# Kernel tuning notes

Hardware: AMD Instinct MI355X
Metric: run time of the kernel (lower is better)

The kernel has to match this reference:

```python
import jax, jax.numpy as jnp
import numpy as np
from jax import lax


def _conv(x, w, b, pad):
    y = lax.conv_general_dilated(x, w, (1, 1), [(pad, pad), (pad, pad)],
                                 dimension_numbers=('NCHW', 'OIHW', 'NCHW'))
    return y + b[None, :, None, None]


def setup_inputs() -> dict:
    key = jax.random.key(0)
    ks = jax.random.split(key, 16)
    B, H, W = 8, 1024, 1024

    def wt(k, shape):
        fan = int(np.prod(shape[1:]))
        return jax.random.normal(k, shape, jnp.float32) / np.sqrt(fan)

    return {
        'x': jax.random.uniform(ks[0], (B, 3, H, W), jnp.float32),
        'w1': wt(ks[1], (3, 3, 1, 1)),  'b1': 0.05 * jax.random.normal(ks[2], (3,), jnp.float32),
        'w2': wt(ks[3], (3, 3, 3, 3)),  'b2': 0.05 * jax.random.normal(ks[4], (3,), jnp.float32),
        'w3': wt(ks[5], (3, 6, 5, 5)),  'b3': 0.05 * jax.random.normal(ks[6], (3,), jnp.float32),
        'w4': wt(ks[7], (3, 6, 7, 7)),  'b4': 0.05 * jax.random.normal(ks[8], (3,), jnp.float32),
        'w5': wt(ks[9], (3, 12, 3, 3)), 'b5': 0.05 * jax.random.normal(ks[10], (3,), jnp.float32),
        'rw1': wt(ks[11], (8, 3, 3, 3)), 'rb1': 0.05 * jax.random.normal(ks[12], (8,), jnp.float32),
        'rw2': wt(ks[13], (3, 8, 3, 3)), 'rb2': 0.05 * jax.random.normal(ks[14], (3,), jnp.float32),
    }


def reference(x, w1, b1, w2, b2, w3, b3, w4, b4, w5, b5, rw1, rb1, rw2, rb2):
    B, _, H, W = x.shape
    relu = jax.nn.relu
    x = jnp.clip(x, 0.0, 1.0)
    original = x

    # K-estimation trunk
    x1 = relu(_conv(x, w1, b1, 0))
    x2 = relu(_conv(x1, w2, b2, 1))
    x3 = relu(_conv(jnp.concatenate([x1, x2], 1), w3, b3, 2))
    x4 = relu(_conv(jnp.concatenate([x2, x3], 1), w4, b4, 3))
    k = relu(_conv(jnp.concatenate([x1, x2, x3, x4], 1), w5, b5, 1))
    k = jnp.clip(k, 0.05, 2.0)

    bright = x.mean(axis=1).reshape(B, -1)           # [B, HW]
    nb = max(int(H * W * 0.001), 1)
    _, idx = lax.top_k(bright, nb)                   # [B, nb]
    flat_img = x.transpose(0, 2, 3, 1).reshape(B, -1, 3)
    A = jnp.take_along_axis(flat_img, idx[:, :, None], axis=1).mean(axis=1)  # [B,3]
    overall = x.mean(axis=(1, 2, 3))
    A = A * jnp.clip(1.2 - overall, 0.8, 1.5)[:, None]
    A = jnp.clip(A, 0.5, 0.95)[:, :, None, None]     # [B,3,1,1]

    # Adaptive transmission and scene radiance recovery
    brightness = x.mean(axis=1, keepdims=True)
    strength = jnp.clip(1.0 - brightness, 0.3, 0.8)
    t = jnp.clip(1.0 - strength * k, 0.1, 1.0)
    J = (x - A) / (t + 1e-5) + A
    J = jnp.nan_to_num(J, nan=0.5, posinf=1.0, neginf=0.0)

    # refinement residual
    refined = _conv(relu(_conv(J, rw1, rb1, 1)), rw2, rb2, 1)
    result = J + 0.2 * refined

    # 'guided filter' loop: the window means are computed but unused; the
    # actual output is a 50/50 blend with the original input.
    result = 0.5 * result + 0.5 * original

    # Histogram equalization per (image, channel) with 256 bins over [0,1]
    ch = result.reshape(B * 3, H * W)
    valid = ((ch >= 0.0) & (ch <= 1.0)).astype(ch.dtype)   # histc ignores out-of-range
    bins = jnp.clip(jnp.floor(ch * 256.0).astype(jnp.int32), 0, 255)
    hist = jax.vmap(lambda b_, v_: jnp.zeros((256,), ch.dtype).at[b_].add(v_))(bins, valid)
    cdf = jnp.cumsum(hist, axis=1)
    lut = jnp.clip(cdf / cdf[:, -1:], 0.0, 1.0)            # [B*3, 256]
    lidx = jnp.clip((ch * 255.0).astype(jnp.int32), 0, 255)
    result = jnp.take_along_axis(lut, lidx, axis=1).reshape(B, 3, H, W)

    # Per-channel contrast stretch
    mn = result.min(axis=(2, 3), keepdims=True)
    mx = result.max(axis=(2, 3), keepdims=True)
    stretch = (result - mn) / jnp.maximum(mx - mn, 0.05) * 0.95
    result = jnp.where(mx - mn > 0.05, stretch, result)

    # Saturation boost + soft contrast curve
    mean_color = result.mean(axis=1, keepdims=True)
    result = mean_color + 1.3 * (result - mean_color)
    result = jax.nn.sigmoid((result - 0.5) * 5.0) * 0.95 + 0.025
    return jnp.clip(result, 0.0, 1.0)
```

## Files before the change

kernel.cpp:

```cpp
#include <hip/hip_runtime.h>
#include <math.h>

#define NBATCH 8
#define IH 1024
#define IW 1024
#define HW (IH*IW)
#define NTOP 1048
#define TIE_CAP 4096

#define TTS 18
#define TD1 (TTS+14)
#define TD2 (TTS+12)
#define TD3 (TTS+8)
#define TD4 (TTS+2)
#define SD1 33
#define SD2 31
#define SD3 27
#define SD4 21
#define CH1 (SD1*TD1+4)
#define CH2 (SD2*TD2+4)
#define CH3 (SD3*TD3+4)
#define CH4 (SD4*TD4+4)

#define RTS 32
#define RD1 (RTS+4)
#define RD2 (RTS+2)

__device__ __forceinline__ float clip01(float v){ return fminf(fmaxf(v, 0.f), 1.f); }

template<int CH,int SD,int KS,int CIN>
__device__ __forceinline__ void accrow4(float a[3][4], const float (*sx)[CH],
    int base, const float* __restrict__ w, int ci0)
{
#pragma unroll 1
  for (int ci = 0; ci < 3; ++ci) {
#pragma unroll 1
    for (int ky = 0; ky < KS; ++ky) {
      float v[KS+3];
      const float* row = &sx[ci][base + ky*SD];
#pragma unroll
      for (int j = 0; j < KS+3; ++j) v[j] = row[j];
#pragma unroll
      for (int o = 0; o < 3; ++o) {
        const float* wp = w + ((o*CIN + ci0+ci)*KS + ky)*KS;
#pragma unroll
        for (int kx = 0; kx < KS; ++kx) {
          float wv = wp[kx];
#pragma unroll
          for (int q = 0; q < 4; ++q)
            a[o][q] = fmaf(v[kx+q], wv, a[o][q]);
        }
      }
    }
  }
}

__global__ void k_init(unsigned* hr, unsigned* prefix, unsigned* remain,
                       float* overall, unsigned* tie_cnt, float* sum_gt,
                       unsigned* histeq, unsigned* mnb, unsigned* mxb)
{
  int t = threadIdx.x;
  for (int i = t; i < 4*NBATCH*256; i += 256) hr[i] = 0u;
  for (int i = t; i < NBATCH*3*256; i += 256) histeq[i] = 0u;
  if (t < NBATCH) { prefix[t] = 0u; remain[t] = NTOP; overall[t] = 0.f; tie_cnt[t] = 0u; }
  if (t < NBATCH*3) { sum_gt[t] = 0.f; mnb[t] = 0x7f7fffffu; mxb[t] = 0u; }
}

__global__ __launch_bounds__(256) void k_bright(const float* __restrict__ x,
    float* __restrict__ bright, float* __restrict__ overall)
{
  __shared__ float sred[256];
  const int b = blockIdx.y;
  const int t = threadIdx.x;
  const float4* c0 = (const float4*)(x + (size_t)b*3*HW);
  const float4* c1 = (const float4*)(x + (size_t)b*3*HW + HW);
  const float4* c2 = (const float4*)(x + (size_t)b*3*HW + 2*(size_t)HW);
  float4* bp = (float4*)(bright + (size_t)b*HW);
  float lsum = 0.f;
  int stride = gridDim.x*blockDim.x;
  for (int i = blockIdx.x*blockDim.x + t; i < HW/4; i += stride) {
    float4 a = c0[i], d = c1[i], e = c2[i];
    float4 br;
    br.x = (clip01(a.x)+clip01(d.x)+clip01(e.x))/3.f;
    br.y = (clip01(a.y)+clip01(d.y)+clip01(e.y))/3.f;
    br.z = (clip01(a.z)+clip01(d.z)+clip01(e.z))/3.f;
    br.w = (clip01(a.w)+clip01(d.w)+clip01(e.w))/3.f;
    bp[i] = br;
    lsum += br.x+br.y+br.z+br.w;
  }
  sred[t] = lsum; __syncthreads();
  for (int s = 128; s > 0; s >>= 1) { if (t < s) sred[t] += sred[t+s]; __syncthreads(); }
  if (t == 0) atomicAdd(&overall[b], sred[0]);
}

__global__ __launch_bounds__(256) void k_trunk(const float* __restrict__ x,
    const float* __restrict__ w1, const float* __restrict__ b1,
    const float* __restrict__ w2, const float* __restrict__ b2,
    const float* __restrict__ w3, const float* __restrict__ b3,
    const float* __restrict__ w4, const float* __restrict__ b4,
    const float* __restrict__ w5, const float* __restrict__ b5,
    float* __restrict__ kout)
{
  __shared__ float s1[3][CH1];
  __shared__ float s2[3][CH2];
  __shared__ float s3[3][CH3];
  __shared__ float s4[3][CH4];
  const int b = blockIdx.z;
  const int gy0 = blockIdx.y*TTS, gx0 = blockIdx.x*TTS;
  const float* xb = x + (size_t)b*3*HW;
  const int tid = threadIdx.x;

  for (int idx = tid; idx < TD1*TD1; idx += 256) {
    int iy = idx/TD1, ix = idx - iy*TD1;
    int gy = gy0 - 7 + iy, gx = gx0 - 7 + ix;
    float o0 = 0.f, o1 = 0.f, o2 = 0.f;
    if (gy >= 0 && gy < IH && gx >= 0 && gx < IW) {
      int gi = gy*IW + gx;
      float c0 = clip01(xb[gi]), c1 = clip01(xb[HW+gi]), c2 = clip01(xb[2*HW+gi]);
      o0 = fmaxf(fmaf(w1[0],c0,fmaf(w1[1],c1,fmaf(w1[2],c2,b1[0]))), 0.f);
      o1 = fmaxf(fmaf(w1[3],c0,fmaf(w1[4],c1,fmaf(w1[5],c2,b1[1]))), 0.f);
      o2 = fmaxf(fmaf(w1[6],c0,fmaf(w1[7],c1,fmaf(w1[8],c2,b1[2]))), 0.f);
    }
    int off = iy*SD1 + ix;
    s1[0][off]=o0; s1[1][off]=o1; s1[2][off]=o2;
  }
  __syncthreads();

  {
    const int NU = ((TD2+3)/4)*TD2;
    int u = tid;
    if (u < NU) {
      int iy = u % TD2, ix0 = (u / TD2)*4;
      int gy = gy0 - 6 + iy;
      float a[3][4];
#pragma unroll
      for (int o=0;o<3;++o){float bv=b2[o];a[o][0]=bv;a[o][1]=bv;a[o][2]=bv;a[o][3]=bv;}
      accrow4<CH1,SD1,3,3>(a, s1, iy*SD1 + ix0, w2, 0);
      bool rowok = (gy >= 0 && gy < IH);
#pragma unroll
      for (int q=0;q<4;++q) {
        int ix = ix0+q;
        if (ix < TD2) {
          int gx = gx0 - 6 + ix;
          bool ok = rowok && gx >= 0 && gx < IW;
          int off = iy*SD2 + ix;
          s2[0][off] = ok ? fmaxf(a[0][q],0.f) : 0.f;
          s2[1][off] = ok ? fmaxf(a[1][q],0.f) : 0.f;
          s2[2][off] = ok ? fmaxf(a[2][q],0.f) : 0.f;
        }
      }
    }
  }
  __syncthreads();

  {
    const int NU = ((TD3+3)/4)*TD3;
    int u = tid;
    if (u < NU) {
      int iy = u % TD3, ix0 = (u / TD3)*4;
      int gy = gy0 - 4 + iy;
      float a[3][4];
#pragma unroll
      for (int o=0;o<3;++o){float bv=b3[o];a[o][0]=bv;a[o][1]=bv;a[o][2]=bv;a[o][3]=bv;}
      accrow4<CH1,SD1,5,6>(a, s1, (iy+1)*SD1 + (ix0+1), w3, 0);
      accrow4<CH2,SD2,5,6>(a, s2, iy*SD2 + ix0,         w3, 3);
      bool rowok = (gy >= 0 && gy < IH);
#pragma unroll
      for (int q=0;q<4;++q) {
        int ix = ix0+q;
        if (ix < TD3) {
          int gx = gx0 - 4 + ix;
          bool ok = rowok && gx >= 0 && gx < IW;
          int off = iy*SD3 + ix;
          s3[0][off] = ok ? fmaxf(a[0][q],0.f) : 0.f;
          s3[1][off] = ok ? fmaxf(a[1][q],0.f) : 0.f;
          s3[2][off] = ok ? fmaxf(a[2][q],0.f) : 0.f;
        }
      }
    }
  }
  __syncthreads();

  {
    const int NU = ((TD4+3)/4)*TD4;
    int u = tid;
    if (u < NU) {
      int iy = u % TD4, ix0 = (u / TD4)*4;
      int gy = gy0 - 1 + iy;
      float a[3][4];
#pragma unroll
      for (int o=0;o<3;++o){float bv=b4[o];a[o][0]=bv;a[o][1]=bv;a[o][2]=bv;a[o][3]=bv;}
      accrow4<CH2,SD2,7,6>(a, s2, (iy+2)*SD2 + (ix0+2), w4, 0);
      accrow4<CH3,SD3,7,6>(a, s3, iy*SD3 + ix0,         w4, 3);
      bool rowok = (gy >= 0 && gy < IH);
#pragma unroll
      for (int q=0;q<4;++q) {
        int ix = ix0+q;
        if (ix < TD4) {
          int gx = gx0 - 1 + ix;
          bool ok = rowok && gx >= 0 && gx < IW;
          int off = iy*SD4 + ix;
          s4[0][off] = ok ? fmaxf(a[0][q],0.f) : 0.f;
          s4[1][off] = ok ? fmaxf(a[1][q],0.f) : 0.f;
          s4[2][off] = ok ? fmaxf(a[2][q],0.f) : 0.f;
        }
      }
    }
  }
  __syncthreads();

  {
    const int NU = ((TTS+3)/4)*TTS;
    int u = tid;
    if (u < NU) {
      int iy = u % TTS, ix0 = (u / TTS)*4;
      int gy = gy0 + iy;
      float a[3][4];
#pragma unroll
      for (int o=0;o<3;++o){float bv=b5[o];a[o][0]=bv;a[o][1]=bv;a[o][2]=bv;a[o][3]=bv;}
      accrow4<CH1,SD1,3,12>(a, s1, (iy+6)*SD1 + (ix0+6), w5, 0);
      accrow4<CH2,SD2,3,12>(a, s2, (iy+5)*SD2 + (ix0+5), w5, 3);
      accrow4<CH3,SD3,3,12>(a, s3, (iy+3)*SD3 + (ix0+3), w5, 6);
      accrow4<CH4,SD4,3,12>(a, s4, iy*SD4 + ix0,         w5, 9);
      if (gy < IH) {
#pragma unroll
        for (int q=0;q<4;++q) {
          int ix = ix0+q;
          int gx = gx0 + ix;
          if (ix < TTS && gx < IW) {
            size_t gi = (size_t)gy*IW + gx;
            kout[((size_t)b*3+0)*HW + gi] = fminf(fmaxf(a[0][q], 0.05f), 2.0f);
            kout[((size_t)b*3+1)*HW + gi] = fminf(fmaxf(a[1][q], 0.05f), 2.0f);
            kout[((size_t)b*3+2)*HW + gi] = fminf(fmaxf(a[2][q], 0.05f), 2.0f);
          }
        }
      }
    }
  }
}

__global__ __launch_bounds__(256) void k_radix_hist(const float* __restrict__ bright,
    const unsigned* __restrict__ prefix, unsigned* __restrict__ hr, int pass)
{
  __shared__ unsigned lh[256];
  const int b = blockIdx.y;
  const int t = threadIdx.x;
  lh[t] = 0u; __syncthreads();
  const unsigned pf = prefix[b];
  const unsigned mask = (pass == 0) ? 0u : (0xFFFFFFFFu << (32 - 8*pass));
  const int shift = 24 - 8*pass;
  const float* br = bright + (size_t)b*HW;
  int stride = gridDim.x*blockDim.x;
  for (int i = blockIdx.x*blockDim.x + t; i < HW; i += stride) {
    unsigned bits = __float_as_uint(br[i]);
    if ((bits & mask) == pf) atomicAdd(&lh[(bits >> shift) & 0xFFu], 1u);
  }
  __syncthreads();
  if (lh[t]) atomicAdd(&hr[(pass*NBATCH + b)*256 + t], lh[t]);
}

__global__ void k_radix_scan(const unsigned* __restrict__ hr,
    unsigned* __restrict__ prefix, unsigned* __restrict__ remain, int pass)
{
  int b = threadIdx.x;
  if (b >= NBATCH) return;
  unsigned rem = remain[b];
  const unsigned* h = hr + (pass*NBATCH + b)*256;
  const int shift = 24 - 8*pass;
  for (int bin = 255; bin >= 0; --bin) {
    unsigned c = h[bin];
    if (rem <= c) { prefix[b] |= ((unsigned)bin) << shift; remain[b] = rem; return; }
    rem -= c;
  }
  remain[b] = rem;
}

__global__ __launch_bounds__(256) void k_gather(const float* __restrict__ x,
    const float* __restrict__ bright, const unsigned* __restrict__ prefix,
    float* __restrict__ sum_gt, unsigned* __restrict__ tie_cnt, unsigned* __restrict__ tie_idx)
{
  const int b = blockIdx.y;
  const unsigned T = prefix[b];
  const float* br = bright + (size_t)b*HW;
  int stride = gridDim.x*blockDim.x;
  for (int i = blockIdx.x*blockDim.x + threadIdx.x; i < HW; i += stride) {
    unsigned bits = __float_as_uint(br[i]);
    if (bits > T) {
#pragma unroll
      for (int c = 0; c < 3; ++c)
        atomicAdd(&sum_gt[b*3+c], clip01(x[((size_t)b*3+c)*HW + i]));
    } else if (bits == T) {
      unsigned p = atomicAdd(&tie_cnt[b], 1u);
      if (p < TIE_CAP) tie_idx[b*TIE_CAP + p] = i;
    }
  }
}

__global__ __launch_bounds__(256) void k_afinal(const float* __restrict__ x,
    const float* __restrict__ sum_gt, const unsigned* __restrict__ tie_cnt,
    const unsigned* __restrict__ tie_idx, const unsigned* __restrict__ remain,
    const float* __restrict__ overall, float* __restrict__ A)
{
  __shared__ unsigned sidx[TIE_CAP];
  __shared__ unsigned sred[256];
  __shared__ float ssum[3];
  const int b = blockIdx.x;
  const int t = threadIdx.x;
  unsigned cnt = tie_cnt[b]; if (cnt > TIE_CAP) cnt = TIE_CAP;
  unsigned need = remain[b]; if (need > cnt) need = cnt;
  if (t < 3) ssum[t] = 0.f;
  for (unsigned i = t; i < cnt; i += 256) sidx[i] = tie_idx[b*TIE_CAP + i];
  __syncthreads();
  if (need == cnt) {
    float l0=0.f,l1=0.f,l2=0.f;
    for (unsigned i = t; i < cnt; i += 256) {
      unsigned px = sidx[i];
      l0 += clip01(x[((size_t)b*3+0)*HW + px]);
      l1 += clip01(x[((size_t)b*3+1)*HW + px]);
      l2 += clip01(x[((size_t)b*3+2)*HW + px]);
    }
    atomicAdd(&ssum[0], l0); atomicAdd(&ssum[1], l1); atomicAdd(&ssum[2], l2);
    __syncthreads();
  } else {
    for (unsigned it = 0; it < need; ++it) {
      unsigned lmin = 0xFFFFFFFFu;
      for (unsigned i = t; i < cnt; i += 256) lmin = min(lmin, sidx[i]);
      sred[t] = lmin; __syncthreads();
      for (int s = 128; s > 0; s >>= 1) { if (t < s) sred[t] = min(sred[t], sred[t+s]); __syncthreads(); }
      unsigned mv = sred[0];
      if (t == 0) {
        ssum[0] += clip01(x[((size_t)b*3+0)*HW + mv]);
        ssum[1] += clip01(x[((size_t)b*3+1)*HW + mv]);
        ssum[2] += clip01(x[((size_t)b*3+2)*HW + mv]);
      }
      for (unsigned i = t; i < cnt; i += 256) if (sidx[i] == mv) sidx[i] = 0xFFFFFFFFu;
      __syncthreads();
    }
  }
  __syncthreads();
  if (t < 3) {
    float a = (sum_gt[b*3+t] + ssum[t]) / (float)NTOP;
    float f = fminf(fmaxf(1.2f - overall[b]/(float)HW, 0.8f), 1.5f);
    A[b*3+t] = fminf(fmaxf(a*f, 0.5f), 0.95f);
  }
}

__global__ __launch_bounds__(256) void k_refineJ(const float* __restrict__ x,
    const float* __restrict__ kin, const float* __restrict__ A,
    const float* __restrict__ rw1, const float* __restrict__ rb1,
    const float* __restrict__ rw2, const float* __restrict__ rb2,
    float* __restrict__ out)
{
  __shared__ float sJ[3][RD1*RD1];
  __shared__ float sH[8][RD2*RD2];
  const int b = blockIdx.z;
  const int gy0 = blockIdx.y*RTS, gx0 = blockIdx.x*RTS;
  const int tid = threadIdx.x;
  const float A0 = A[b*3+0], A1 = A[b*3+1], A2 = A[b*3+2];
  const float* xb = x + (size_t)b*3*HW;
  const float* kb = kin + (size_t)b*3*HW;

  for (int idx = tid; idx < RD1*RD1; idx += 256) {
    int iy = idx/RD1, ix = idx - iy*RD1;
    int gy = gy0 - 2 + iy, gx = gx0 - 2 + ix;
    float j0 = 0.f, j1 = 0.f, j2 = 0.f;
    if (gy >= 0 && gy < IH && gx >= 0 && gx < IW) {
      size_t gi = (size_t)gy*IW + gx;
      float c0 = clip01(xb[gi]), c1 = clip01(xb[HW+gi]), c2 = clip01(xb[2*(size_t)HW+gi]);
      float br = (c0+c1+c2)/3.f;
      float st = fminf(fmaxf(1.f-br, 0.3f), 0.8f);
      float t0 = fminf(fmaxf(1.f-st*kb[gi],             0.1f),1.f)+1e-5f;
      float t1 = fminf(fmaxf(1.f-st*kb[HW+gi],          0.1f),1.f)+1e-5f;
      float t2 = fminf(fmaxf(1.f-st*kb[2*(size_t)HW+gi],0.1f),1.f)+1e-5f;
      j0 = (c0-A0)/t0 + A0;
      j1 = (c1-A1)/t1 + A1;
      j2 = (c2-A2)/t2 + A2;
    }
    sJ[0][idx]=j0; sJ[1][idx]=j1; sJ[2][idx]=j2;
  }
  __syncthreads();

  for (int idx = tid; idx < RD2*RD2; idx += 256) {
    int iy = idx/RD2, ix = idx - iy*RD2;
    int gy = gy0 - 1 + iy, gx = gx0 - 1 + ix;
    float acc[8];
#pragma unroll
    for (int o = 0; o < 8; ++o) acc[o] = rb1[o];
    if (gy >= 0 && gy < IH && gx >= 0 && gx < IW) {
#pragma unroll
      for (int ci = 0; ci < 3; ++ci) {
#pragma unroll
        for (int ky = 0; ky < 3; ++ky) {
#pragma unroll
          for (int kx = 0; kx < 3; ++kx) {
            float v = sJ[ci][(iy+ky)*RD1 + ix+kx];
#pragma unroll
            for (int o = 0; o < 8; ++o)
              acc[o] = fmaf(v, rw1[((o*3+ci)*3+ky)*3+kx], acc[o]);
          }
        }
      }
#pragma unroll
      for (int o = 0; o < 8; ++o) sH[o][idx] = fmaxf(acc[o], 0.f);
    } else {
#pragma unroll
      for (int o = 0; o < 8; ++o) sH[o][idx] = 0.f;
    }
  }
  __syncthreads();

  for (int idx = tid; idx < RTS*RTS; idx += 256) {
    int iy = idx/RTS, ix = idx - iy*RTS;
    int gy = gy0 + iy, gx = gx0 + ix;
    float r0 = rb2[0], r1 = rb2[1], r2 = rb2[2];
#pragma unroll
    for (int ci = 0; ci < 8; ++ci) {
#pragma unroll
      for (int ky = 0; ky < 3; ++ky) {
#pragma unroll
        for (int kx = 0; kx < 3; ++kx) {
          float v = sH[ci][(iy+ky)*RD2 + ix+kx];
          r0 = fmaf(v, rw2[((0*8+ci)*3+ky)*3+kx], r0);
          r1 = fmaf(v, rw2[((1*8+ci)*3+ky)*3+kx], r1);
          r2 = fmaf(v, rw2[((2*8+ci)*3+ky)*3+kx], r2);
        }
      }
    }
    size_t gi = (size_t)gy*IW + gx;
    float j0 = sJ[0][(iy+2)*RD1 + ix+2];
    float j1 = sJ[1][(iy+2)*RD1 + ix+2];
    float j2 = sJ[2][(iy+2)*RD1 + ix+2];
    out[((size_t)b*3+0)*HW + gi] = 0.5f*(j0 + 0.2f*r0) + 0.5f*clip01(xb[gi]);
    out[((size_t)b*3+1)*HW + gi] = 0.5f*(j1 + 0.2f*r1) + 0.5f*clip01(xb[HW+gi]);
    out[((size_t)b*3+2)*HW + gi] = 0.5f*(j2 + 0.2f*r2) + 0.5f*clip01(xb[2*(size_t)HW+gi]);
  }
}

__global__ __launch_bounds__(256) void k_hist(const float* __restrict__ r, unsigned* __restrict__ hist)
{
  __shared__ unsigned lh[256];
  const int slice = blockIdx.y;
  const int t = threadIdx.x;
  lh[t] = 0u; __syncthreads();
  const float4* p = (const float4*)(r + (size_t)slice*HW);
  int stride = gridDim.x*blockDim.x;
  for (int i = blockIdx.x*blockDim.x + t; i < HW/4; i += stride) {
    float4 v = p[i];
    float a[4] = {v.x, v.y, v.z, v.w};
#pragma unroll
    for (int q = 0; q < 4; ++q) {
      float vv = a[q];
      if (vv >= 0.f && vv <= 1.f) {
        int bin = (int)floorf(vv*256.f);
        bin = min(max(bin, 0), 255);
        atomicAdd(&lh[bin], 1u);
      }
    }
  }
  __syncthreads();
  if (lh[t]) atomicAdd(&hist[slice*256 + t], lh[t]);
}

__global__ void k_cdf(const unsigned* __restrict__ hist, float* __restrict__ lut)
{
  __shared__ float sc[256];
  const int s = blockIdx.x;
  const int t = threadIdx.x;
  sc[t] = (float)hist[s*256 + t];
  __syncthreads();
  for (int off = 1; off < 256; off <<= 1) {
    float add = (t >= off) ? sc[t-off] : 0.f;
    __syncthreads();
    sc[t] += add;
    __syncthreads();
  }
  float total = sc[255];
  lut[s*256 + t] = fminf(fmaxf(sc[t]/total, 0.f), 1.f);
}

__global__ __launch_bounds__(256) void k_apply(float* r, const float* __restrict__ lut,
    unsigned* __restrict__ mnb, unsigned* __restrict__ mxb)
{
  __shared__ float slut[256];
  __shared__ float smn[256], smx[256];
  const int slice = blockIdx.y;
  const int t = threadIdx.x;
  slut[t] = lut[slice*256 + t];
  __syncthreads();
  float lmn = 3.4e38f, lmx = -3.4e38f;
  float4* p = (float4*)(r + (size_t)slice*HW);
  int stride = gridDim.x*blockDim.x;
  for (int i = blockIdx.x*blockDim.x + t; i < HW/4; i += stride) {
    float4 v = p[i];
    float o0 = slut[min(max((int)(v.x*255.f), 0), 255)];
    float o1 = slut[min(max((int)(v.y*255.f), 0), 255)];
    float o2 = slut[min(max((int)(v.z*255.f), 0), 255)];
    float o3 = slut[min(max((int)(v.w*255.f), 0), 255)];
    lmn = fminf(lmn, fminf(fminf(o0,o1), fminf(o2,o3)));
    lmx = fmaxf(lmx, fmaxf(fmaxf(o0,o1), fmaxf(o2,o3)));
    float4 ov = {o0,o1,o2,o3};
    p[i] = ov;
  }
  smn[t] = lmn; smx[t] = lmx; __syncthreads();
  for (int s = 128; s > 0; s >>= 1) {
    if (t < s) { smn[t] = fminf(smn[t], smn[t+s]); smx[t] = fmaxf(smx[t], smx[t+s]); }
    __syncthreads();
  }
  if (t == 0) {
    atomicMin(&mnb[slice], __float_as_uint(smn[0]));
    atomicMax(&mxb[slice], __float_as_uint(smx[0]));
  }
}

__global__ __launch_bounds__(256) void k_final(float* r,
    const unsigned* __restrict__ mnb, const unsigned* __restrict__ mxb)
{
  const int b = blockIdx.y;
  float mn[3], mx[3];
#pragma unroll
  for (int c = 0; c < 3; ++c) { mn[c] = __uint_as_float(mnb[b*3+c]); mx[c] = __uint_as_float(mxb[b*3+c]); }
  int stride = gridDim.x*blockDim.x;
  for (int i = blockIdx.x*blockDim.x + threadIdx.x; i < HW/4; i += stride) {
    float4 v[3];
#pragma unroll
    for (int c = 0; c < 3; ++c) v[c] = ((const float4*)(r + ((size_t)b*3+c)*HW))[i];
    float* f0 = (float*)&v[0]; float* f1 = (float*)&v[1]; float* f2 = (float*)&v[2];
#pragma unroll
    for (int q = 0; q < 4; ++q) {
      float rr[3] = { f0[q], f1[q], f2[q] };
#pragma unroll
      for (int c = 0; c < 3; ++c) {
        float d = mx[c] - mn[c];
        if (d > 0.05f) rr[c] = (rr[c] - mn[c]) / fmaxf(d, 0.05f) * 0.95f;
      }
      float m = (rr[0] + rr[1] + rr[2]) / 3.f;
#pragma unroll
      for (int c = 0; c < 3; ++c) {
        float s = m + 1.3f*(rr[c] - m);
        float o = 1.f/(1.f + expf(-(s - 0.5f)*5.f))*0.95f + 0.025f;
        rr[c] = clip01(o);
      }
      f0[q] = rr[0]; f1[q] = rr[1]; f2[q] = rr[2];
    }
#pragma unroll
    for (int c = 0; c < 3; ++c) ((float4*)(r + ((size_t)b*3+c)*HW))[i] = v[c];
  }
}

extern "C" void kernel_launch(void* const* d_in, const int* in_sizes, int n_in,
                              void* d_out, int out_size, void* d_ws, size_t ws_size,
                              hipStream_t stream) {
  const float* x   = (const float*)d_in[0];
  const float* w1  = (const float*)d_in[1];  const float* b1 = (const float*)d_in[2];
  const float* w2  = (const float*)d_in[3];  const float* b2 = (const float*)d_in[4];
  const float* w3  = (const float*)d_in[5];  const float* b3 = (const float*)d_in[6];
  const float* w4  = (const float*)d_in[7];  const float* b4 = (const float*)d_in[8];
  const float* w5  = (const float*)d_in[9];  const float* b5 = (const float*)d_in[10];
  const float* rw1 = (const float*)d_in[11]; const float* rb1 = (const float*)d_in[12];
  const float* rw2 = (const float*)d_in[13]; const float* rb2 = (const float*)d_in[14];
  float* out = (float*)d_out;

  float* ws = (float*)d_ws;
  float* kbuf   = ws;
  float* bright = kbuf + (size_t)NBATCH*3*HW;
  float* overall = bright + (size_t)NBATCH*HW;
  float* sum_gt  = overall + NBATCH;
  float* Abuf    = sum_gt + NBATCH*3;
  float* lut     = Abuf + NBATCH*3;
  unsigned* hr      = (unsigned*)(lut + NBATCH*3*256);
  unsigned* prefix  = hr + 4*NBATCH*256;
  unsigned* remain  = prefix + NBATCH;
  unsigned* tie_cnt = remain + NBATCH;
  unsigned* tie_idx = tie_cnt + NBATCH;
  unsigned* histeq  = tie_idx + NBATCH*TIE_CAP;
  unsigned* mnb     = histeq + NBATCH*3*256;
  unsigned* mxb     = mnb + NBATCH*3;

  k_init<<<1, 256, 0, stream>>>(hr, prefix, remain, overall, tie_cnt, sum_gt, histeq, mnb, mxb);
  k_bright<<<dim3(1024, NBATCH), 256, 0, stream>>>(x, bright, overall);
  k_trunk<<<dim3((IW+TTS-1)/TTS, (IH+TTS-1)/TTS, NBATCH), 256, 0, stream>>>(
      x, w1, b1, w2, b2, w3, b3, w4, b4, w5, b5, kbuf);
  for (int p = 0; p < 4; ++p) {
    k_radix_hist<<<dim3(64, NBATCH), 256, 0, stream>>>(bright, prefix, hr, p);
    k_radix_scan<<<1, 64, 0, stream>>>(hr, prefix, remain, p);
  }
  k_gather<<<dim3(128, NBATCH), 256, 0, stream>>>(x, bright, prefix, sum_gt, tie_cnt, tie_idx);
  k_afinal<<<NBATCH, 256, 0, stream>>>(x, sum_gt, tie_cnt, tie_idx, remain, overall, Abuf);
  k_refineJ<<<dim3(IW/RTS, IH/RTS, NBATCH), 256, 0, stream>>>(
      x, kbuf, Abuf, rw1, rb1, rw2, rb2, out);
  k_hist<<<dim3(64, NBATCH*3), 256, 0, stream>>>(out, histeq);
  k_cdf<<<NBATCH*3, 256, 0, stream>>>(histeq, lut);
  k_apply<<<dim3(64, NBATCH*3), 256, 0, stream>>>(out, lut, mnb, mxb);
  k_final<<<dim3(128, NBATCH), 256, 0, stream>>>(out, mnb, mxb);
}
```

Measured before the change: 1.852 ms.

## Vectorize trunk shared-memory access with float4-aligned tiles and 16-pixel output tiles

```diff
diff --git a/kernel.cpp b/kernel.cpp
--- a/kernel.cpp
+++ b/kernel.cpp
@@ -8,19 +8,19 @@
 #define NTOP 1048
 #define TIE_CAP 4096
 
-#define TTS 18
+#define TTS 16
 #define TD1 (TTS+14)
 #define TD2 (TTS+12)
 #define TD3 (TTS+8)
 #define TD4 (TTS+2)
-#define SD1 33
-#define SD2 31
-#define SD3 27
-#define SD4 21
-#define CH1 (SD1*TD1+4)
-#define CH2 (SD2*TD2+4)
-#define CH3 (SD3*TD3+4)
-#define CH4 (SD4*TD4+4)
+#define SDU1 9
+#define SDU2 7
+#define SDU3 7
+#define SDU4 5
+#define CH1 (SDU1*4*TD1+16)
+#define CH2 (SDU2*4*TD2+16)
+#define CH3 (SDU3*4*TD3+16)
+#define CH4 (SDU4*4*TD4+16)
 
 #define RTS 32
 #define RD1 (RTS+4)
@@ -28,18 +28,26 @@
 
 __device__ __forceinline__ float clip01(float v){ return fminf(fmaxf(v, 0.f), 1.f); }
 
-template<int CH,int SD,int KS,int CIN>
+template<int CH,int SDU,int KS,int CIN,int DROW,int DCOL>
 __device__ __forceinline__ void accrow4(float a[3][4], const float (*sx)[CH],
-    int base, const float* __restrict__ w, int ci0)
-{
+    int iy, int ix0, const float* __restrict__ w, int ci0)
+{
+  constexpr int PH = DCOL & 3;
+  constexpr int NU = (PH + KS + 3 + 3) >> 2;
 #pragma unroll 1
   for (int ci = 0; ci < 3; ++ci) {
+    const float4* chan = (const float4*)(&sx[ci][0]);
+    const int ub = (iy + DROW) * SDU + (ix0 >> 2) + (DCOL >> 2);
 #pragma unroll 1
     for (int ky = 0; ky < KS; ++ky) {
-      float v[KS+3];
-      const float* row = &sx[ci][base + ky*SD];
-#pragma unroll
-      for (int j = 0; j < KS+3; ++j) v[j] = row[j];
+      float4 qv[NU];
+#pragma unroll
+      for (int uu = 0; uu < NU; ++uu) qv[uu] = chan[ub + ky*SDU + uu];
+      float vv[NU*4];
+#pragma unroll
+      for (int uu = 0; uu < NU; ++uu) {
+        vv[4*uu+0]=qv[uu].x; vv[4*uu+1]=qv[uu].y; vv[4*uu+2]=qv[uu].z; vv[4*uu+3]=qv[uu].w;
+      }
 #pragma unroll
       for (int o = 0; o < 3; ++o) {
         const float* wp = w + ((o*CIN + ci0+ci)*KS + ky)*KS;
@@ -47,12 +55,22 @@
         for (int kx = 0; kx < KS; ++kx) {
           float wv = wp[kx];
 #pragma unroll
-          for (int q = 0; q < 4; ++q)
-            a[o][q] = fmaf(v[kx+q], wv, a[o][q]);
+          for (int qq = 0; qq < 4; ++qq)
+            a[o][qq] = fmaf(vv[PH + kx + qq], wv, a[o][qq]);
         }
       }
     }
   }
+}
+
+__device__ __forceinline__ float4 sel4(const float a[4], bool rowok, int gxs, int ixs, int tdlim)
+{
+  float4 r;
+  r.x = (rowok && (unsigned)(gxs+0) < IW && (ixs+0) < tdlim) ? fmaxf(a[0],0.f) : 0.f;
+  r.y = (rowok && (unsigned)(gxs+1) < IW && (ixs+1) < tdlim) ? fmaxf(a[1],0.f) : 0.f;
+  r.z = (rowok && (unsigned)(gxs+2) < IW && (ixs+2) < tdlim) ? fmaxf(a[2],0.f) : 0.f;
+  r.w = (rowok && (unsigned)(gxs+3) < IW && (ixs+3) < tdlim) ? fmaxf(a[3],0.f) : 0.f;
+  return r;
 }
 
 __global__ void k_init(unsigned* hr, unsigned* prefix, unsigned* remain,
@@ -101,10 +119,10 @@
     const float* __restrict__ w5, const float* __restrict__ b5,
     float* __restrict__ kout)
 {
-  __shared__ float s1[3][CH1];
-  __shared__ float s2[3][CH2];
-  __shared__ float s3[3][CH3];
-  __shared__ float s4[3][CH4];
+  __shared__ __align__(16) float s1[3][CH1];
+  __shared__ __align__(16) float s2[3][CH2];
+  __shared__ __align__(16) float s3[3][CH3];
+  __shared__ __align__(16) float s4[3][CH4];
   const int b = blockIdx.z;
   const int gy0 = blockIdx.y*TTS, gx0 = blockIdx.x*TTS;
   const float* xb = x + (size_t)b*3*HW;
@@ -121,120 +139,86 @@
       o1 = fmaxf(fmaf(w1[3],c0,fmaf(w1[4],c1,fmaf(w1[5],c2,b1[1]))), 0.f);
       o2 = fmaxf(fmaf(w1[6],c0,fmaf(w1[7],c1,fmaf(w1[8],c2,b1[2]))), 0.f);
     }
-    int off = iy*SD1 + ix;
+    int off = iy*(SDU1*4) + ix;
     s1[0][off]=o0; s1[1][off]=o1; s1[2][off]=o2;
   }
   __syncthreads();
 
-  {
-    const int NU = ((TD2+3)/4)*TD2;
-    int u = tid;
-    if (u < NU) {
-      int iy = u % TD2, ix0 = (u / TD2)*4;
-      int gy = gy0 - 6 + iy;
-      float a[3][4];
-#pragma unroll
-      for (int o=0;o<3;++o){float bv=b2[o];a[o][0]=bv;a[o][1]=bv;a[o][2]=bv;a[o][3]=bv;}
-      accrow4<CH1,SD1,3,3>(a, s1, iy*SD1 + ix0, w2, 0);
-      bool rowok = (gy >= 0 && gy < IH);
-#pragma unroll
-      for (int q=0;q<4;++q) {
-        int ix = ix0+q;
-        if (ix < TD2) {
-          int gx = gx0 - 6 + ix;
-          bool ok = rowok && gx >= 0 && gx < IW;
-          int off = iy*SD2 + ix;
-          s2[0][off] = ok ? fmaxf(a[0][q],0.f) : 0.f;
-          s2[1][off] = ok ? fmaxf(a[1][q],0.f) : 0.f;
-          s2[2][off] = ok ? fmaxf(a[2][q],0.f) : 0.f;
-        }
-      }
-    }
-  }
-  __syncthreads();
-
-  {
-    const int NU = ((TD3+3)/4)*TD3;
-    int u = tid;
-    if (u < NU) {
-      int iy = u % TD3, ix0 = (u / TD3)*4;
-      int gy = gy0 - 4 + iy;
-      float a[3][4];
-#pragma unroll
-      for (int o=0;o<3;++o){float bv=b3[o];a[o][0]=bv;a[o][1]=bv;a[o][2]=bv;a[o][3]=bv;}
-      accrow4<CH1,SD1,5,6>(a, s1, (iy+1)*SD1 + (ix0+1), w3, 0);
-      accrow4<CH2,SD2,5,6>(a, s2, iy*SD2 + ix0,         w3, 3);
-      bool rowok = (gy >= 0 && gy < IH);
-#pragma unroll
-      for (int q=0;q<4;++q) {
-        int ix = ix0+q;
-        if (ix < TD3) {
-          int gx = gx0 - 4 + ix;
-          bool ok = rowok && gx >= 0 && gx < IW;
-          int off = iy*SD3 + ix;
-          s3[0][off] = ok ? fmaxf(a[0][q],0.f) : 0.f;
-          s3[1][off] = ok ? fmaxf(a[1][q],0.f) : 0.f;
-          s3[2][off] = ok ? fmaxf(a[2][q],0.f) : 0.f;
-        }
-      }
-    }
-  }
-  __syncthreads();
-
-  {
-    const int NU = ((TD4+3)/4)*TD4;
-    int u = tid;
-    if (u < NU) {
-      int iy = u % TD4, ix0 = (u / TD4)*4;
-      int gy = gy0 - 1 + iy;
-      float a[3][4];
-#pragma unroll
-      for (int o=0;o<3;++o){float bv=b4[o];a[o][0]=bv;a[o][1]=bv;a[o][2]=bv;a[o][3]=bv;}
-      accrow4<CH2,SD2,7,6>(a, s2, (iy+2)*SD2 + (ix0+2), w4, 0);
-      accrow4<CH3,SD3,7,6>(a, s3, iy*SD3 + ix0,         w4, 3);
-      bool rowok = (gy >= 0 && gy < IH);
-#pragma unroll
-      for (int q=0;q<4;++q) {
-        int ix = ix0+q;
-        if (ix < TD4) {
-          int gx = gx0 - 1 + ix;
-          bool ok = rowok && gx >= 0 && gx < IW;
-          int off = iy*SD4 + ix;
-          s4[0][off] = ok ? fmaxf(a[0][q],0.f) : 0.f;
-          s4[1][off] = ok ? fmaxf(a[1][q],0.f) : 0.f;
-          s4[2][off] = ok ? fmaxf(a[2][q],0.f) : 0.f;
-        }
-      }
-    }
-  }
-  __syncthreads();
-
-  {
-    const int NU = ((TTS+3)/4)*TTS;
-    int u = tid;
-    if (u < NU) {
-      int iy = u % TTS, ix0 = (u / TTS)*4;
-      int gy = gy0 + iy;
-      float a[3][4];
-#pragma unroll
-      for (int o=0;o<3;++o){float bv=b5[o];a[o][0]=bv;a[o][1]=bv;a[o][2]=bv;a[o][3]=bv;}
-      accrow4<CH1,SD1,3,12>(a, s1, (iy+6)*SD1 + (ix0+6), w5, 0);
-      accrow4<CH2,SD2,3,12>(a, s2, (iy+5)*SD2 + (ix0+5), w5, 3);
-      accrow4<CH3,SD3,3,12>(a, s3, (iy+3)*SD3 + (ix0+3), w5, 6);
-      accrow4<CH4,SD4,3,12>(a, s4, iy*SD4 + ix0,         w5, 9);
-      if (gy < IH) {
-#pragma unroll
-        for (int q=0;q<4;++q) {
-          int ix = ix0+q;
-          int gx = gx0 + ix;
-          if (ix < TTS && gx < IW) {
-            size_t gi = (size_t)gy*IW + gx;
-            kout[((size_t)b*3+0)*HW + gi] = fminf(fmaxf(a[0][q], 0.05f), 2.0f);
-            kout[((size_t)b*3+1)*HW + gi] = fminf(fmaxf(a[1][q], 0.05f), 2.0f);
-            kout[((size_t)b*3+2)*HW + gi] = fminf(fmaxf(a[2][q], 0.05f), 2.0f);
-          }
-        }
-      }
+  if (tid < 7*TD2) {
+    int iy = tid % TD2, ix0 = (tid / TD2)*4;
+    int gy = gy0 - 6 + iy;
+    float a[3][4];
+#pragma unroll
+    for (int o=0;o<3;++o){float bv=b2[o];a[o][0]=bv;a[o][1]=bv;a[o][2]=bv;a[o][3]=bv;}
+    accrow4<CH1,SDU1,3,3,0,0>(a, s1, iy, ix0, w2, 0);
+    bool rowok = (gy >= 0 && gy < IH);
+    int off = iy*(SDU2*4) + ix0;
+    float4 v0 = sel4(a[0], rowok, gx0-6+ix0, ix0, TD2);
+    float4 v1 = sel4(a[1], rowok, gx0-6+ix0, ix0, TD2);
+    float4 v2 = sel4(a[2], rowok, gx0-6+ix0, ix0, TD2);
+    *(float4*)&s2[0][off] = v0;
+    *(float4*)&s2[1][off] = v1;
+    *(float4*)&s2[2][off] = v2;
+  }
+  __syncthreads();
+
+  if (tid < 6*TD3) {
+    int iy = tid % TD3, ix0 = (tid / TD3)*4;
+    int gy = gy0 - 4 + iy;
+    float a[3][4];
+#pragma unroll
+    for (int o=0;o<3;++o){float bv=b3[o];a[o][0]=bv;a[o][1]=bv;a[o][2]=bv;a[o][3]=bv;}
+    accrow4<CH1,SDU1,5,6,1,1>(a, s1, iy, ix0, w3, 0);
+    accrow4<CH2,SDU2,5,6,0,0>(a, s2, iy, ix0, w3, 3);
+    bool rowok = (gy >= 0 && gy < IH);
+    int off = iy*(SDU3*4) + ix0;
+    float4 v0 = sel4(a[0], rowok, gx0-4+ix0, ix0, TD3);
+    float4 v1 = sel4(a[1], rowok, gx0-4+ix0, ix0, TD3);
+    float4 v2 = sel4(a[2], rowok, gx0-4+ix0, ix0, TD3);
+    *(float4*)&s3[0][off] = v0;
+    *(float4*)&s3[1][off] = v1;
+    *(float4*)&s3[2][off] = v2;
+  }
+  __syncthreads();
+
+  if (tid < 5*TD4) {
+    int iy = tid % TD4, ix0 = (tid / TD4)*4;
+    int gy = gy0 - 1 + iy;
+    float a[3][4];
+#pragma unroll
+    for (int o=0;o<3;++o){float bv=b4[o];a[o][0]=bv;a[o][1]=bv;a[o][2]=bv;a[o][3]=bv;}
+    accrow4<CH2,SDU2,7,6,2,2>(a, s2, iy, ix0, w4, 0);
+    accrow4<CH3,SDU3,7,6,0,0>(a, s3, iy, ix0, w4, 3);
+    bool rowok = (gy >= 0 && gy < IH);
+    int off = iy*(SDU4*4) + ix0;
+    float4 v0 = sel4(a[0], rowok, gx0-1+ix0, ix0, TD4);
+    float4 v1 = sel4(a[1], rowok, gx0-1+ix0, ix0, TD4);
+    float4 v2 = sel4(a[2], rowok, gx0-1+ix0, ix0, TD4);
+    *(float4*)&s4[0][off] = v0;
+    *(float4*)&s4[1][off] = v1;
+    *(float4*)&s4[2][off] = v2;
+  }
+  __syncthreads();
+
+  if (tid < 4*TTS) {
+    int iy = tid % TTS, ix0 = (tid / TTS)*4;
+    int gy = gy0 + iy;
+    float a[3][4];
+#pragma unroll
+    for (int o=0;o<3;++o){float bv=b5[o];a[o][0]=bv;a[o][1]=bv;a[o][2]=bv;a[o][3]=bv;}
+    accrow4<CH1,SDU1,3,12,6,6>(a, s1, iy, ix0, w5, 0);
+    accrow4<CH2,SDU2,3,12,5,5>(a, s2, iy, ix0, w5, 3);
+    accrow4<CH3,SDU3,3,12,3,3>(a, s3, iy, ix0, w5, 6);
+    accrow4<CH4,SDU4,3,12,0,0>(a, s4, iy, ix0, w5, 9);
+    size_t gi = (size_t)gy*IW + (gx0 + ix0);
+#pragma unroll
+    for (int o = 0; o < 3; ++o) {
+      float4 kv;
+      kv.x = fminf(fmaxf(a[o][0], 0.05f), 2.0f);
+      kv.y = fminf(fmaxf(a[o][1], 0.05f), 2.0f);
+      kv.z = fminf(fmaxf(a[o][2], 0.05f), 2.0f);
+      kv.w = fminf(fmaxf(a[o][3], 0.05f), 2.0f);
+      *(float4*)&kout[((size_t)b*3+o)*HW + gi] = kv;
     }
   }
 }
@@ -578,7 +562,7 @@
 
   k_init<<<1, 256, 0, stream>>>(hr, prefix, remain, overall, tie_cnt, sum_gt, histeq, mnb, mxb);
   k_bright<<<dim3(1024, NBATCH), 256, 0, stream>>>(x, bright, overall);
-  k_trunk<<<dim3((IW+TTS-1)/TTS, (IH+TTS-1)/TTS, NBATCH), 256, 0, stream>>>(
+  k_trunk<<<dim3(IW/TTS, IH/TTS, NBATCH), 256, 0, stream>>>(
       x, w1, b1, w2, b2, w3, b3, w4, b4, w5, b5, kbuf);
   for (int p = 0; p < 4; ++p) {
     k_radix_hist<<<dim3(64, NBATCH), 256, 0, stream>>>(bright, prefix, hr, p);
```

Result: slower. 1.989 ms (+7.4%).
